# Optimization experiments

Measured on AMD Instinct MI355X. Metric: run time of the kernel, lower is better.

## Reference

```python
import jax, jax.numpy as jnp
import numpy as np

N_NODES = 65536


def gcn_conv(x, W, b, src, dst, n_nodes):
    """PyG GCNConv: symmetric-normalized aggregation with self-loops.
    out = D^{-1/2} (A + I) D^{-1/2} (x W) + b, deg counted on targets incl. self-loop.
    """
    h = x @ W  # [N, F_out]
    # in-degree including the self-loop
    deg = jnp.zeros((n_nodes,), dtype=x.dtype).at[dst].add(1.0) + 1.0
    dis = jax.lax.rsqrt(deg)  # deg^{-1/2}
    norm = dis[src] * dis[dst]  # [E]
    msg = h[src] * norm[:, None]  # [E, F_out] gathered+scaled messages
    agg = jax.ops.segment_sum(msg, dst, num_segments=n_nodes)
    agg = agg + h * (dis * dis)[:, None]  # self-loop contribution, norm = dis[i]^2
    return agg + b


def setup_inputs() -> dict:
    key = jax.random.key(0)
    k1, k2, k3, k4 = jax.random.split(key, 4)
    d_in, d_hid = 64, 64
    x = jax.random.normal(k1, (N_NODES, d_in), dtype=jnp.float32)
    edge_index = jax.random.randint(k2, (2, 1048576), 0, N_NODES, dtype=jnp.int64)
    s = 1.0 / np.sqrt(d_in)
    W1 = jax.random.normal(k3, (d_in, d_hid), dtype=jnp.float32) * s
    b1 = jnp.zeros((d_hid,), dtype=jnp.float32)
    W2 = jax.random.normal(k4, (d_hid, d_hid), dtype=jnp.float32) * s
    b2 = jnp.zeros((d_hid,), dtype=jnp.float32)
    return {"x": x, "edge_index": edge_index, "W1": W1, "b1": b1, "W2": W2, "b2": b2}


def reference(x, edge_index, W1, b1, W2, b2):
    src, dst = edge_index[0], edge_index[1]
    n = x.shape[0]
    h = jax.nn.relu(gcn_conv(x, W1, b1, src, dst, n))
    h = jax.nn.relu(gcn_conv(h, W2, b2, src, dst, n))
    return h
```

## Files before the change

kernel.cpp:

```cpp
#include <hip/hip_runtime.h>

#define FDIM 64
#define EPB  1024
#define BCAP 6144

typedef float nf4 __attribute__((ext_vector_type(4)));
typedef float nf2 __attribute__((ext_vector_type(2)));

__device__ __forceinline__ unsigned f2bf(float f) {
    unsigned u = __float_as_uint(f);
    u += 0x7fffu + ((u >> 16) & 1u);
    return u >> 16;
}
__device__ __forceinline__ float bflo(unsigned u) { return __uint_as_float(u << 16); }
__device__ __forceinline__ float bfhi(unsigned u) { return __uint_as_float(u & 0xffff0000u); }


__global__ __launch_bounds__(256) void k_coarse(const int* __restrict__ ei,
                                                int* __restrict__ cursorG,
                                                int* __restrict__ packed, int nE) {
    __shared__ int lh[256], gb[256], lc[256];
    int t = threadIdx.x;
    lh[t] = 0; lc[t] = 0;
    __syncthreads();
    int base = blockIdx.x * EPB;
    int bins[EPB / 256], vals[EPB / 256];
    #pragma unroll
    for (int i = 0; i < EPB / 256; ++i) {
        int e = base + i * 256 + t;
        if (e < nE) {
            int s = ei[e];
            int d = ei[nE + e];
            bins[i] = d >> 8;
            vals[i] = (s << 8) | (d & 255);
            atomicAdd(&lh[bins[i]], 1);
        } else {
            bins[i] = -1;
        }
    }
    __syncthreads();
    gb[t] = atomicAdd(&cursorG[t], lh[t]);
    __syncthreads();
    #pragma unroll
    for (int i = 0; i < EPB / 256; ++i) {
        int b = bins[i];
        if (b >= 0) {
            int p = gb[b] + atomicAdd(&lc[b], 1);
            if (p < BCAP) packed[b * BCAP + p] = vals[i];
        }
    }
}

__global__ __launch_bounds__(256) void k_fine(const int* __restrict__ packed,
                                              const int* __restrict__ cursorG,
                                              float* __restrict__ dis,
                                              int* __restrict__ rowStart,
                                              unsigned short* __restrict__ lenArr,
                                              unsigned short* __restrict__ sortedSrc,
                                              int n) {
    __shared__ int cnt[256], loc[256], lc[256];
    int t = threadIdx.x;
    int b = blockIdx.x;
    int lo = b * BCAP;
    int hi = lo + cursorG[b];
    cnt[t] = 0; lc[t] = 0;
    __syncthreads();
    for (int k = lo + t; k < hi; k += 256)
        atomicAdd(&cnt[packed[k] & 255], 1);
    __syncthreads();

    int c = cnt[t];
    int node = (b << 8) + t;
    dis[node]    = rsqrtf((float)c + 1.0f);
    lenArr[node] = (unsigned short)c;

    loc[t] = c;
    __syncthreads();
    #pragma unroll
    for (int off = 1; off < 256; off <<= 1) {
        int u = (t >= off) ? loc[t - off] : 0;
        __syncthreads();
        loc[t] += u;
        __syncthreads();
    }
    int excl = loc[t] - c;
    rowStart[node] = lo + excl;
    __syncthreads();
    loc[t] = excl;
    __syncthreads();

    for (int k = lo + t; k < hi; k += 256) {
        int v = packed[k];
        int dl = v & 255;
        int p = loc[dl] + atomicAdd(&lc[dl], 1);
        sortedSrc[lo + p] = (unsigned short)(v >> 8);
    }
}


__global__ __launch_bounds__(256) void k_gemm64s(const float* __restrict__ X,
                                                 const float* __restrict__ W,
                                                 const float* __restrict__ dis,
                                                 unsigned* __restrict__ Hb) {
    __shared__ float Ws[64 * 64];
    __shared__ float XsT[64 * 68];

    const int tid  = threadIdx.x;
    const int row0 = blockIdx.x * 64;

    for (int i = tid; i < 4096; i += 256) Ws[i] = W[i];
    for (int i = tid; i < 4096; i += 256) {
        int r = i >> 6, k = i & 63;
        XsT[k * 68 + r] = X[(row0 + r) * FDIM + k];
    }
    __syncthreads();

    const int tx = tid & 15;
    const int ty = tid >> 4;

    float4 acc0 = {0,0,0,0}, acc1 = {0,0,0,0}, acc2 = {0,0,0,0}, acc3 = {0,0,0,0};

    #pragma unroll
    for (int k = 0; k < 64; ++k) {
        float4 wv = *(const float4*)&Ws[k * 64 + tx * 4];
        float4 xv = *(const float4*)&XsT[k * 68 + ty * 4];
        acc0.x = fmaf(xv.x, wv.x, acc0.x); acc0.y = fmaf(xv.x, wv.y, acc0.y);
        acc0.z = fmaf(xv.x, wv.z, acc0.z); acc0.w = fmaf(xv.x, wv.w, acc0.w);
        acc1.x = fmaf(xv.y, wv.x, acc1.x); acc1.y = fmaf(xv.y, wv.y, acc1.y);
        acc1.z = fmaf(xv.y, wv.z, acc1.z); acc1.w = fmaf(xv.y, wv.w, acc1.w);
        acc2.x = fmaf(xv.z, wv.x, acc2.x); acc2.y = fmaf(xv.z, wv.y, acc2.y);
        acc2.z = fmaf(xv.z, wv.z, acc2.z); acc2.w = fmaf(xv.z, wv.w, acc2.w);
        acc3.x = fmaf(xv.w, wv.x, acc3.x); acc3.y = fmaf(xv.w, wv.y, acc3.y);
        acc3.z = fmaf(xv.w, wv.z, acc3.z); acc3.w = fmaf(xv.w, wv.w, acc3.w);
    }

    float d0 = dis[row0 + ty * 4 + 0];
    float d1 = dis[row0 + ty * 4 + 1];
    float d2 = dis[row0 + ty * 4 + 2];
    float d3 = dis[row0 + ty * 4 + 3];

    uint2* H2 = (uint2*)Hb;
    uint2 o;
    o.x = f2bf(acc0.x * d0) | (f2bf(acc0.y * d0) << 16);
    o.y = f2bf(acc0.z * d0) | (f2bf(acc0.w * d0) << 16);
    H2[(row0 + ty * 4 + 0) * 16 + tx] = o;
    o.x = f2bf(acc1.x * d1) | (f2bf(acc1.y * d1) << 16);
    o.y = f2bf(acc1.z * d1) | (f2bf(acc1.w * d1) << 16);
    H2[(row0 + ty * 4 + 1) * 16 + tx] = o;
    o.x = f2bf(acc2.x * d2) | (f2bf(acc2.y * d2) << 16);
    o.y = f2bf(acc2.z * d2) | (f2bf(acc2.w * d2) << 16);
    H2[(row0 + ty * 4 + 2) * 16 + tx] = o;
    o.x = f2bf(acc3.x * d3) | (f2bf(acc3.y * d3) << 16);
    o.y = f2bf(acc3.z * d3) | (f2bf(acc3.w * d3) << 16);
    H2[(row0 + ty * 4 + 3) * 16 + tx] = o;
}


__global__ __launch_bounds__(256) void k_aggemm(const unsigned* __restrict__ Hb1,
                                                const float* __restrict__ dis,
                                                const int* __restrict__ rowStart,
                                                const unsigned short* __restrict__ lenArr,
                                                const unsigned short* __restrict__ esrc,
                                                const float* __restrict__ bias,
                                                const float* __restrict__ W,
                                                unsigned* __restrict__ Hb2) {
    __shared__ float Ws[64 * 64];
    __shared__ float XsT[64 * 68];

    const int tid  = threadIdx.x;
    const int row0 = blockIdx.x * 64;

    for (int i = tid; i < 4096; i += 256) Ws[i] = W[i];

    const int fq = tid & 7;
    const int rr = tid >> 3;
    const uint4* H = (const uint4*)Hb1;
    const float4* b4 = (const float4*)bias;
    const float4 bb0 = b4[fq * 2];
    const float4 bb1 = b4[fq * 2 + 1];

    #pragma unroll
    for (int half = 0; half < 2; ++half) {
        const int r   = rr + half * 32;
        const int row = row0 + r;
        const int start = rowStart[row];
        const int end   = start + (int)lenArr[row];

        nf2 p0 = {0, 0}, p1 = {0, 0}, p2 = {0, 0}, p3 = {0, 0};
        int k = start;
        for (; k + 4 <= end; k += 4) {
            int s0 = (int)__builtin_nontemporal_load(&esrc[k]);
            int s1 = (int)__builtin_nontemporal_load(&esrc[k + 1]);
            int s2 = (int)__builtin_nontemporal_load(&esrc[k + 2]);
            int s3 = (int)__builtin_nontemporal_load(&esrc[k + 3]);
            uint4 v0 = H[s0 * 8 + fq];
            uint4 v1 = H[s1 * 8 + fq];
            uint4 v2 = H[s2 * 8 + fq];
            uint4 v3 = H[s3 * 8 + fq];
            p0 += (nf2){bflo(v0.x), bfhi(v0.x)}; p1 += (nf2){bflo(v0.y), bfhi(v0.y)};
            p2 += (nf2){bflo(v0.z), bfhi(v0.z)}; p3 += (nf2){bflo(v0.w), bfhi(v0.w)};
            p0 += (nf2){bflo(v1.x), bfhi(v1.x)}; p1 += (nf2){bflo(v1.y), bfhi(v1.y)};
            p2 += (nf2){bflo(v1.z), bfhi(v1.z)}; p3 += (nf2){bflo(v1.w), bfhi(v1.w)};
            p0 += (nf2){bflo(v2.x), bfhi(v2.x)}; p1 += (nf2){bflo(v2.y), bfhi(v2.y)};
            p2 += (nf2){bflo(v2.z), bfhi(v2.z)}; p3 += (nf2){bflo(v2.w), bfhi(v2.w)};
            p0 += (nf2){bflo(v3.x), bfhi(v3.x)}; p1 += (nf2){bflo(v3.y), bfhi(v3.y)};
            p2 += (nf2){bflo(v3.z), bfhi(v3.z)}; p3 += (nf2){bflo(v3.w), bfhi(v3.w)};
        }
        for (; k < end; ++k) {
            int s0 = (int)__builtin_nontemporal_load(&esrc[k]);
            uint4 v0 = H[s0 * 8 + fq];
            p0 += (nf2){bflo(v0.x), bfhi(v0.x)}; p1 += (nf2){bflo(v0.y), bfhi(v0.y)};
            p2 += (nf2){bflo(v0.z), bfhi(v0.z)}; p3 += (nf2){bflo(v0.w), bfhi(v0.w)};
        }

        uint4 sv = H[row * 8 + fq];
        float ds = dis[row];
        float* col = &XsT[(fq * 8) * 68 + r];
        col[0 * 68] = fmaxf(fmaf(p0.x + bflo(sv.x), ds, bb0.x), 0.f);
        col[1 * 68] = fmaxf(fmaf(p0.y + bfhi(sv.x), ds, bb0.y), 0.f);
        col[2 * 68] = fmaxf(fmaf(p1.x + bflo(sv.y), ds, bb0.z), 0.f);
        col[3 * 68] = fmaxf(fmaf(p1.y + bfhi(sv.y), ds, bb0.w), 0.f);
        col[4 * 68] = fmaxf(fmaf(p2.x + bflo(sv.z), ds, bb1.x), 0.f);
        col[5 * 68] = fmaxf(fmaf(p2.y + bfhi(sv.z), ds, bb1.y), 0.f);
        col[6 * 68] = fmaxf(fmaf(p3.x + bflo(sv.w), ds, bb1.z), 0.f);
        col[7 * 68] = fmaxf(fmaf(p3.y + bfhi(sv.w), ds, bb1.w), 0.f);
    }
    __syncthreads();

    const int tx = tid & 15;
    const int ty = tid >> 4;

    float4 acc0 = {0,0,0,0}, acc1 = {0,0,0,0}, acc2 = {0,0,0,0}, acc3 = {0,0,0,0};

    #pragma unroll
    for (int k = 0; k < 64; ++k) {
        float4 wv = *(const float4*)&Ws[k * 64 + tx * 4];
        float4 xv = *(const float4*)&XsT[k * 68 + ty * 4];
        acc0.x = fmaf(xv.x, wv.x, acc0.x); acc0.y = fmaf(xv.x, wv.y, acc0.y);
        acc0.z = fmaf(xv.x, wv.z, acc0.z); acc0.w = fmaf(xv.x, wv.w, acc0.w);
        acc1.x = fmaf(xv.y, wv.x, acc1.x); acc1.y = fmaf(xv.y, wv.y, acc1.y);
        acc1.z = fmaf(xv.y, wv.z, acc1.z); acc1.w = fmaf(xv.y, wv.w, acc1.w);
        acc2.x = fmaf(xv.z, wv.x, acc2.x); acc2.y = fmaf(xv.z, wv.y, acc2.y);
        acc2.z = fmaf(xv.z, wv.z, acc2.z); acc2.w = fmaf(xv.z, wv.w, acc2.w);
        acc3.x = fmaf(xv.w, wv.x, acc3.x); acc3.y = fmaf(xv.w, wv.y, acc3.y);
        acc3.z = fmaf(xv.w, wv.z, acc3.z); acc3.w = fmaf(xv.w, wv.w, acc3.w);
    }

    float d0 = dis[row0 + ty * 4 + 0];
    float d1 = dis[row0 + ty * 4 + 1];
    float d2 = dis[row0 + ty * 4 + 2];
    float d3 = dis[row0 + ty * 4 + 3];

    uint2* H2 = (uint2*)Hb2;
    uint2 o;
    o.x = f2bf(acc0.x * d0) | (f2bf(acc0.y * d0) << 16);
    o.y = f2bf(acc0.z * d0) | (f2bf(acc0.w * d0) << 16);
    H2[(row0 + ty * 4 + 0) * 16 + tx] = o;
    o.x = f2bf(acc1.x * d1) | (f2bf(acc1.y * d1) << 16);
    o.y = f2bf(acc1.z * d1) | (f2bf(acc1.w * d1) << 16);
    H2[(row0 + ty * 4 + 1) * 16 + tx] = o;
    o.x = f2bf(acc2.x * d2) | (f2bf(acc2.y * d2) << 16);
    o.y = f2bf(acc2.z * d2) | (f2bf(acc2.w * d2) << 16);
    H2[(row0 + ty * 4 + 2) * 16 + tx] = o;
    o.x = f2bf(acc3.x * d3) | (f2bf(acc3.y * d3) << 16);
    o.y = f2bf(acc3.z * d3) | (f2bf(acc3.w * d3) << 16);
    H2[(row0 + ty * 4 + 3) * 16 + tx] = o;
}


__global__ __launch_bounds__(256) void k_agg(const unsigned* __restrict__ Hb,
                                             const float* __restrict__ dis,
                                             const int* __restrict__ rowStart,
                                             const unsigned short* __restrict__ lenArr,
                                             const unsigned short* __restrict__ esrc,
                                             const float* __restrict__ bias,
                                             float* __restrict__ out) {
    const int tid = threadIdx.x;
    const int fq  = tid & 7;
    const int row = blockIdx.x * 32 + (tid >> 3);

    const int start = rowStart[row];
    const int end   = start + (int)lenArr[row];

    const uint4* H = (const uint4*)Hb;

    nf2 p0 = {0, 0}, p1 = {0, 0}, p2 = {0, 0}, p3 = {0, 0};

    int k = start;
    for (; k + 4 <= end; k += 4) {
        int s0 = (int)__builtin_nontemporal_load(&esrc[k]);
        int s1 = (int)__builtin_nontemporal_load(&esrc[k + 1]);
        int s2 = (int)__builtin_nontemporal_load(&esrc[k + 2]);
        int s3 = (int)__builtin_nontemporal_load(&esrc[k + 3]);
        uint4 v0 = H[s0 * 8 + fq];
        uint4 v1 = H[s1 * 8 + fq];
        uint4 v2 = H[s2 * 8 + fq];
        uint4 v3 = H[s3 * 8 + fq];
        p0 += (nf2){bflo(v0.x), bfhi(v0.x)}; p1 += (nf2){bflo(v0.y), bfhi(v0.y)};
        p2 += (nf2){bflo(v0.z), bfhi(v0.z)}; p3 += (nf2){bflo(v0.w), bfhi(v0.w)};
        p0 += (nf2){bflo(v1.x), bfhi(v1.x)}; p1 += (nf2){bflo(v1.y), bfhi(v1.y)};
        p2 += (nf2){bflo(v1.z), bfhi(v1.z)}; p3 += (nf2){bflo(v1.w), bfhi(v1.w)};
        p0 += (nf2){bflo(v2.x), bfhi(v2.x)}; p1 += (nf2){bflo(v2.y), bfhi(v2.y)};
        p2 += (nf2){bflo(v2.z), bfhi(v2.z)}; p3 += (nf2){bflo(v2.w), bfhi(v2.w)};
        p0 += (nf2){bflo(v3.x), bfhi(v3.x)}; p1 += (nf2){bflo(v3.y), bfhi(v3.y)};
        p2 += (nf2){bflo(v3.z), bfhi(v3.z)}; p3 += (nf2){bflo(v3.w), bfhi(v3.w)};
    }
    for (; k < end; ++k) {
        int s0 = (int)__builtin_nontemporal_load(&esrc[k]);
        uint4 v0 = H[s0 * 8 + fq];
        p0 += (nf2){bflo(v0.x), bfhi(v0.x)}; p1 += (nf2){bflo(v0.y), bfhi(v0.y)};
        p2 += (nf2){bflo(v0.z), bfhi(v0.z)}; p3 += (nf2){bflo(v0.w), bfhi(v0.w)};
    }

    uint4 sv = H[row * 8 + fq];
    float ds = dis[row];
    const float4* b4 = (const float4*)bias;
    float4 b0 = b4[fq * 2];
    float4 b1 = b4[fq * 2 + 1];

    nf4 r0, r1;
    r0.x = fmaxf(fmaf(p0.x + bflo(sv.x), ds, b0.x), 0.f);
    r0.y = fmaxf(fmaf(p0.y + bfhi(sv.x), ds, b0.y), 0.f);
    r0.z = fmaxf(fmaf(p1.x + bflo(sv.y), ds, b0.z), 0.f);
    r0.w = fmaxf(fmaf(p1.y + bfhi(sv.y), ds, b0.w), 0.f);
    r1.x = fmaxf(fmaf(p2.x + bflo(sv.z), ds, b1.x), 0.f);
    r1.y = fmaxf(fmaf(p2.y + bfhi(sv.z), ds, b1.y), 0.f);
    r1.z = fmaxf(fmaf(p3.x + bflo(sv.w), ds, b1.z), 0.f);
    r1.w = fmaxf(fmaf(p3.y + bfhi(sv.w), ds, b1.w), 0.f);

    nf4* O = (nf4*)out;
    __builtin_nontemporal_store(r0, &O[row * 16 + fq * 2]);
    __builtin_nontemporal_store(r1, &O[row * 16 + fq * 2 + 1]);
}


extern "C" void kernel_launch(void* const* d_in, const int* in_sizes, int n_in,
                              void* d_out, int out_size, void* d_ws, size_t ws_size,
                              hipStream_t stream) {
    const float* x  = (const float*)d_in[0];
    const int*   ei = (const int*)d_in[1];
    const float* W1 = (const float*)d_in[2];
    const float* b1 = (const float*)d_in[3];
    const float* W2 = (const float*)d_in[4];
    const float* b2 = (const float*)d_in[5];

    const int N = in_sizes[0] / FDIM;
    const int E = in_sizes[1] / 2;

    char* ws = (char*)d_ws;
    float*          dis       = (float*)(ws);
    int*            rowStart  = (int*)  (ws + 262144);
    unsigned short* lenArr    = (unsigned short*)(ws + 524288);
    int*            cursorG   = (int*)  (ws + 655360);
    unsigned short* sortedSrc = (unsigned short*)(ws + 656384);
    char*           heap      = ws + 656384 + 3145728;
    int*            packed    = (int*)heap;
    unsigned*       HSb1      = (unsigned*)heap;
    unsigned*       HSb2      = (unsigned*)(heap + 8388608);

    hipMemsetAsync(cursorG, 0, 256 * sizeof(int), stream);
    k_coarse<<<(E + EPB - 1) / EPB, 256, 0, stream>>>(ei, cursorG, packed, E);
    k_fine  <<<256, 256, 0, stream>>>(packed, cursorG, dis, rowStart, lenArr, sortedSrc, N);

    k_gemm64s<<<N / 64, 256, 0, stream>>>(x, W1, dis, HSb1);
    k_aggemm <<<N / 64, 256, 0, stream>>>(HSb1, dis, rowStart, lenArr, sortedSrc, b1, W2, HSb2);
    k_agg    <<<N / 32, 256, 0, stream>>>(HSb2, dis, rowStart, lenArr, sortedSrc, b2, (float*)d_out);
}
```

Baseline: 118.0 us.

## Decouple first GEMM from degree computation and fold memset into it

The first-layer GEMM no longer scales rows by deg^-1/2, so it can run before the edge sort. It also absorbs the cursor memset through an extra block, which removes one API call. The aggregation kernels now gather dis[src] per edge and multiply each message by it, and the self-loop term and output are scaled by the destination's dis. This cuts one dependency and one launch at the cost of an extra scalar gather and multiply per edge in both aggregation passes, and the workspace layout is reshuffled so packed no longer aliases H1.

```diff
diff --git a/kernel.cpp b/kernel.cpp
--- a/kernel.cpp
+++ b/kernel.cpp
@@ -14,6 +14,69 @@
 }
 __device__ __forceinline__ float bflo(unsigned u) { return __uint_as_float(u << 16); }
 __device__ __forceinline__ float bfhi(unsigned u) { return __uint_as_float(u & 0xffff0000u); }
+
+#define ACC4(v) \
+    p0 += (nf2){bflo((v).x), bfhi((v).x)}; p1 += (nf2){bflo((v).y), bfhi((v).y)}; \
+    p2 += (nf2){bflo((v).z), bfhi((v).z)}; p3 += (nf2){bflo((v).w), bfhi((v).w)};
+
+
+__global__ __launch_bounds__(256) void k_gemm64u(const float* __restrict__ X,
+                                                 const float* __restrict__ W,
+                                                 unsigned* __restrict__ Hb,
+                                                 int* __restrict__ cursorG,
+                                                 int nTiles) {
+    if ((int)blockIdx.x >= nTiles) {
+        if (threadIdx.x < 256) cursorG[threadIdx.x] = 0;
+        return;
+    }
+    __shared__ float Ws[64 * 64];
+    __shared__ float XsT[64 * 68];
+
+    const int tid  = threadIdx.x;
+    const int row0 = blockIdx.x * 64;
+
+    for (int i = tid; i < 4096; i += 256) Ws[i] = W[i];
+    for (int i = tid; i < 4096; i += 256) {
+        int r = i >> 6, k = i & 63;
+        XsT[k * 68 + r] = X[(row0 + r) * FDIM + k];
+    }
+    __syncthreads();
+
+    const int tx = tid & 15;
+    const int ty = tid >> 4;
+
+    float4 acc0 = {0,0,0,0}, acc1 = {0,0,0,0}, acc2 = {0,0,0,0}, acc3 = {0,0,0,0};
+
+    #pragma unroll
+    for (int k = 0; k < 64; ++k) {
+        float4 wv = *(const float4*)&Ws[k * 64 + tx * 4];
+        float4 xv = *(const float4*)&XsT[k * 68 + ty * 4];
+        acc0.x = fmaf(xv.x, wv.x, acc0.x); acc0.y = fmaf(xv.x, wv.y, acc0.y);
+        acc0.z = fmaf(xv.x, wv.z, acc0.z); acc0.w = fmaf(xv.x, wv.w, acc0.w);
+        acc1.x = fmaf(xv.y, wv.x, acc1.x); acc1.y = fmaf(xv.y, wv.y, acc1.y);
+        acc1.z = fmaf(xv.y, wv.z, acc1.z); acc1.w = fmaf(xv.y, wv.w, acc1.w);
+        acc2.x = fmaf(xv.z, wv.x, acc2.x); acc2.y = fmaf(xv.z, wv.y, acc2.y);
+        acc2.z = fmaf(xv.z, wv.z, acc2.z); acc2.w = fmaf(xv.z, wv.w, acc2.w);
+        acc3.x = fmaf(xv.w, wv.x, acc3.x); acc3.y = fmaf(xv.w, wv.y, acc3.y);
+        acc3.z = fmaf(xv.w, wv.z, acc3.z); acc3.w = fmaf(xv.w, wv.w, acc3.w);
+    }
+
+    uint2* H2 = (uint2*)Hb;
+    uint2 o;
+    o.x = f2bf(acc0.x) | (f2bf(acc0.y) << 16);
+    o.y = f2bf(acc0.z) | (f2bf(acc0.w) << 16);
+    H2[(row0 + ty * 4 + 0) * 16 + tx] = o;
+    o.x = f2bf(acc1.x) | (f2bf(acc1.y) << 16);
+    o.y = f2bf(acc1.z) | (f2bf(acc1.w) << 16);
+    H2[(row0 + ty * 4 + 1) * 16 + tx] = o;
+    o.x = f2bf(acc2.x) | (f2bf(acc2.y) << 16);
+    o.y = f2bf(acc2.z) | (f2bf(acc2.w) << 16);
+    H2[(row0 + ty * 4 + 2) * 16 + tx] = o;
+    o.x = f2bf(acc3.x) | (f2bf(acc3.y) << 16);
+    o.y = f2bf(acc3.z) | (f2bf(acc3.w) << 16);
+    H2[(row0 + ty * 4 + 3) * 16 + tx] = o;
+}
+
 
 
 __global__ __launch_bounds__(256) void k_coarse(const int* __restrict__ ei,
@@ -98,10 +161,14 @@
 }
 
 
-__global__ __launch_bounds__(256) void k_gemm64s(const float* __restrict__ X,
-                                                 const float* __restrict__ W,
-                                                 const float* __restrict__ dis,
-                                                 unsigned* __restrict__ Hb) {
+__global__ __launch_bounds__(256) void k_aggemm(const unsigned* __restrict__ Hb1,
+                                                const float* __restrict__ dis,
+                                                const int* __restrict__ rowStart,
+                                                const unsigned short* __restrict__ lenArr,
+                                                const unsigned short* __restrict__ esrc,
+                                                const float* __restrict__ bias,
+                                                const float* __restrict__ W,
+                                                unsigned* __restrict__ Hb2) {
     __shared__ float Ws[64 * 64];
     __shared__ float XsT[64 * 68];
 
@@ -109,9 +176,71 @@
     const int row0 = blockIdx.x * 64;
 
     for (int i = tid; i < 4096; i += 256) Ws[i] = W[i];
-    for (int i = tid; i < 4096; i += 256) {
-        int r = i >> 6, k = i & 63;
-        XsT[k * 68 + r] = X[(row0 + r) * FDIM + k];
+
+    const int fq = tid & 7;
+    const int rr = tid >> 3;
+    const uint4* H = (const uint4*)Hb1;
+    const float4* b4 = (const float4*)bias;
+    const float4 bb0 = b4[fq * 2];
+    const float4 bb1 = b4[fq * 2 + 1];
+
+    #pragma unroll
+    for (int half = 0; half < 2; ++half) {
+        const int r   = rr + half * 32;
+        const int row = row0 + r;
+        const int start = rowStart[row];
+        const int end   = start + (int)lenArr[row];
+
+        nf2 p0 = {0, 0}, p1 = {0, 0}, p2 = {0, 0}, p3 = {0, 0};
+        int k = start;
+        for (; k + 4 <= end; k += 4) {
+            int s0 = (int)__builtin_nontemporal_load(&esrc[k]);
+            int s1 = (int)__builtin_nontemporal_load(&esrc[k + 1]);
+            int s2 = (int)__builtin_nontemporal_load(&esrc[k + 2]);
+            int s3 = (int)__builtin_nontemporal_load(&esrc[k + 3]);
+            uint4 v0 = H[s0 * 8 + fq];
+            uint4 v1 = H[s1 * 8 + fq];
+            uint4 v2 = H[s2 * 8 + fq];
+            uint4 v3 = H[s3 * 8 + fq];
+            float w0 = dis[s0], w1 = dis[s1], w2 = dis[s2], w3 = dis[s3];
+            p0 += (nf2){bflo(v0.x) * w0, bfhi(v0.x) * w0};
+            p1 += (nf2){bflo(v0.y) * w0, bfhi(v0.y) * w0};
+            p2 += (nf2){bflo(v0.z) * w0, bfhi(v0.z) * w0};
+            p3 += (nf2){bflo(v0.w) * w0, bfhi(v0.w) * w0};
+            p0 += (nf2){bflo(v1.x) * w1, bfhi(v1.x) * w1};
+            p1 += (nf2){bflo(v1.y) * w1, bfhi(v1.y) * w1};
+            p2 += (nf2){bflo(v1.z) * w1, bfhi(v1.z) * w1};
+            p3 += (nf2){bflo(v1.w) * w1, bfhi(v1.w) * w1};
+            p0 += (nf2){bflo(v2.x) * w2, bfhi(v2.x) * w2};
+            p1 += (nf2){bflo(v2.y) * w2, bfhi(v2.y) * w2};
+            p2 += (nf2){bflo(v2.z) * w2, bfhi(v2.z) * w2};
+            p3 += (nf2){bflo(v2.w) * w2, bfhi(v2.w) * w2};
+            p0 += (nf2){bflo(v3.x) * w3, bfhi(v3.x) * w3};
+            p1 += (nf2){bflo(v3.y) * w3, bfhi(v3.y) * w3};
+            p2 += (nf2){bflo(v3.z) * w3, bfhi(v3.z) * w3};
+            p3 += (nf2){bflo(v3.w) * w3, bfhi(v3.w) * w3};
+        }
+        for (; k < end; ++k) {
+            int s0 = (int)__builtin_nontemporal_load(&esrc[k]);
+            uint4 v0 = H[s0 * 8 + fq];
+            float w0 = dis[s0];
+            p0 += (nf2){bflo(v0.x) * w0, bfhi(v0.x) * w0};
+            p1 += (nf2){bflo(v0.y) * w0, bfhi(v0.y) * w0};
+            p2 += (nf2){bflo(v0.z) * w0, bfhi(v0.z) * w0};
+            p3 += (nf2){bflo(v0.w) * w0, bfhi(v0.w) * w0};
+        }
+
+        uint4 sv = H[row * 8 + fq];
+        float ds = dis[row];
+        float* col = &XsT[(fq * 8) * 68 + r];
+        col[0 * 68] = fmaxf(fmaf(fmaf(bflo(sv.x), ds, p0.x), ds, bb0.x), 0.f);
+        col[1 * 68] = fmaxf(fmaf(fmaf(bfhi(sv.x), ds, p0.y), ds, bb0.y), 0.f);
+        col[2 * 68] = fmaxf(fmaf(fmaf(bflo(sv.y), ds, p1.x), ds, bb0.z), 0.f);
+        col[3 * 68] = fmaxf(fmaf(fmaf(bfhi(sv.y), ds, p1.y), ds, bb0.w), 0.f);
+        col[4 * 68] = fmaxf(fmaf(fmaf(bflo(sv.z), ds, p2.x), ds, bb1.x), 0.f);
+        col[5 * 68] = fmaxf(fmaf(fmaf(bfhi(sv.z), ds, p2.y), ds, bb1.y), 0.f);
+        col[6 * 68] = fmaxf(fmaf(fmaf(bflo(sv.w), ds, p3.x), ds, bb1.z), 0.f);
+        col[7 * 68] = fmaxf(fmaf(fmaf(bfhi(sv.w), ds, p3.y), ds, bb1.w), 0.f);
     }
     __syncthreads();
 
@@ -134,136 +263,19 @@
         acc3.z = fmaf(xv.w, wv.z, acc3.z); acc3.w = fmaf(xv.w, wv.w, acc3.w);
     }
 
-    float d0 = dis[row0 + ty * 4 + 0];
-    float d1 = dis[row0 + ty * 4 + 1];
-    float d2 = dis[row0 + ty * 4 + 2];
-    float d3 = dis[row0 + ty * 4 + 3];
-
-    uint2* H2 = (uint2*)Hb;
-    uint2 o;
-    o.x = f2bf(acc0.x * d0) | (f2bf(acc0.y * d0) << 16);
-    o.y = f2bf(acc0.z * d0) | (f2bf(acc0.w * d0) << 16);
-    H2[(row0 + ty * 4 + 0) * 16 + tx] = o;
-    o.x = f2bf(acc1.x * d1) | (f2bf(acc1.y * d1) << 16);
-    o.y = f2bf(acc1.z * d1) | (f2bf(acc1.w * d1) << 16);
-    H2[(row0 + ty * 4 + 1) * 16 + tx] = o;
-    o.x = f2bf(acc2.x * d2) | (f2bf(acc2.y * d2) << 16);
-    o.y = f2bf(acc2.z * d2) | (f2bf(acc2.w * d2) << 16);
-    H2[(row0 + ty * 4 + 2) * 16 + tx] = o;
-    o.x = f2bf(acc3.x * d3) | (f2bf(acc3.y * d3) << 16);
-    o.y = f2bf(acc3.z * d3) | (f2bf(acc3.w * d3) << 16);
-    H2[(row0 + ty * 4 + 3) * 16 + tx] = o;
-}
-
-
-__global__ __launch_bounds__(256) void k_aggemm(const unsigned* __restrict__ Hb1,
-                                                const float* __restrict__ dis,
-                                                const int* __restrict__ rowStart,
-                                                const unsigned short* __restrict__ lenArr,
-                                                const unsigned short* __restrict__ esrc,
-                                                const float* __restrict__ bias,
-                                                const float* __restrict__ W,
-                                                unsigned* __restrict__ Hb2) {
-    __shared__ float Ws[64 * 64];
-    __shared__ float XsT[64 * 68];
-
-    const int tid  = threadIdx.x;
-    const int row0 = blockIdx.x * 64;
-
-    for (int i = tid; i < 4096; i += 256) Ws[i] = W[i];
-
-    const int fq = tid & 7;
-    const int rr = tid >> 3;
-    const uint4* H = (const uint4*)Hb1;
-    const float4* b4 = (const float4*)bias;
-    const float4 bb0 = b4[fq * 2];
-    const float4 bb1 = b4[fq * 2 + 1];
-
-    #pragma unroll
-    for (int half = 0; half < 2; ++half) {
-        const int r   = rr + half * 32;
-        const int row = row0 + r;
-        const int start = rowStart[row];
-        const int end   = start + (int)lenArr[row];
-
-        nf2 p0 = {0, 0}, p1 = {0, 0}, p2 = {0, 0}, p3 = {0, 0};
-        int k = start;
-        for (; k + 4 <= end; k += 4) {
-            int s0 = (int)__builtin_nontemporal_load(&esrc[k]);
-            int s1 = (int)__builtin_nontemporal_load(&esrc[k + 1]);
-            int s2 = (int)__builtin_nontemporal_load(&esrc[k + 2]);
-            int s3 = (int)__builtin_nontemporal_load(&esrc[k + 3]);
-            uint4 v0 = H[s0 * 8 + fq];
-            uint4 v1 = H[s1 * 8 + fq];
-            uint4 v2 = H[s2 * 8 + fq];
-            uint4 v3 = H[s3 * 8 + fq];
-            p0 += (nf2){bflo(v0.x), bfhi(v0.x)}; p1 += (nf2){bflo(v0.y), bfhi(v0.y)};
-            p2 += (nf2){bflo(v0.z), bfhi(v0.z)}; p3 += (nf2){bflo(v0.w), bfhi(v0.w)};
-            p0 += (nf2){bflo(v1.x), bfhi(v1.x)}; p1 += (nf2){bflo(v1.y), bfhi(v1.y)};
-            p2 += (nf2){bflo(v1.z), bfhi(v1.z)}; p3 += (nf2){bflo(v1.w), bfhi(v1.w)};
-            p0 += (nf2){bflo(v2.x), bfhi(v2.x)}; p1 += (nf2){bflo(v2.y), bfhi(v2.y)};
-            p2 += (nf2){bflo(v2.z), bfhi(v2.z)}; p3 += (nf2){bflo(v2.w), bfhi(v2.w)};
-            p0 += (nf2){bflo(v3.x), bfhi(v3.x)}; p1 += (nf2){bflo(v3.y), bfhi(v3.y)};
-            p2 += (nf2){bflo(v3.z), bfhi(v3.z)}; p3 += (nf2){bflo(v3.w), bfhi(v3.w)};
-        }
-        for (; k < end; ++k) {
-            int s0 = (int)__builtin_nontemporal_load(&esrc[k]);
-            uint4 v0 = H[s0 * 8 + fq];
-            p0 += (nf2){bflo(v0.x), bfhi(v0.x)}; p1 += (nf2){bflo(v0.y), bfhi(v0.y)};
-            p2 += (nf2){bflo(v0.z), bfhi(v0.z)}; p3 += (nf2){bflo(v0.w), bfhi(v0.w)};
-        }
-
-        uint4 sv = H[row * 8 + fq];
-        float ds = dis[row];
-        float* col = &XsT[(fq * 8) * 68 + r];
-        col[0 * 68] = fmaxf(fmaf(p0.x + bflo(sv.x), ds, bb0.x), 0.f);
-        col[1 * 68] = fmaxf(fmaf(p0.y + bfhi(sv.x), ds, bb0.y), 0.f);
-        col[2 * 68] = fmaxf(fmaf(p1.x + bflo(sv.y), ds, bb0.z), 0.f);
-        col[3 * 68] = fmaxf(fmaf(p1.y + bfhi(sv.y), ds, bb0.w), 0.f);
-        col[4 * 68] = fmaxf(fmaf(p2.x + bflo(sv.z), ds, bb1.x), 0.f);
-        col[5 * 68] = fmaxf(fmaf(p2.y + bfhi(sv.z), ds, bb1.y), 0.f);
-        col[6 * 68] = fmaxf(fmaf(p3.x + bflo(sv.w), ds, bb1.z), 0.f);
-        col[7 * 68] = fmaxf(fmaf(p3.y + bfhi(sv.w), ds, bb1.w), 0.f);
-    }
-    __syncthreads();
-
-    const int tx = tid & 15;
-    const int ty = tid >> 4;
-
-    float4 acc0 = {0,0,0,0}, acc1 = {0,0,0,0}, acc2 = {0,0,0,0}, acc3 = {0,0,0,0};
-
-    #pragma unroll
-    for (int k = 0; k < 64; ++k) {
-        float4 wv = *(const float4*)&Ws[k * 64 + tx * 4];
-        float4 xv = *(const float4*)&XsT[k * 68 + ty * 4];
-        acc0.x = fmaf(xv.x, wv.x, acc0.x); acc0.y = fmaf(xv.x, wv.y, acc0.y);
-        acc0.z = fmaf(xv.x, wv.z, acc0.z); acc0.w = fmaf(xv.x, wv.w, acc0.w);
-        acc1.x = fmaf(xv.y, wv.x, acc1.x); acc1.y = fmaf(xv.y, wv.y, acc1.y);
-        acc1.z = fmaf(xv.y, wv.z, acc1.z); acc1.w = fmaf(xv.y, wv.w, acc1.w);
-        acc2.x = fmaf(xv.z, wv.x, acc2.x); acc2.y = fmaf(xv.z, wv.y, acc2.y);
-        acc2.z = fmaf(xv.z, wv.z, acc2.z); acc2.w = fmaf(xv.z, wv.w, acc2.w);
-        acc3.x = fmaf(xv.w, wv.x, acc3.x); acc3.y = fmaf(xv.w, wv.y, acc3.y);
-        acc3.z = fmaf(xv.w, wv.z, acc3.z); acc3.w = fmaf(xv.w, wv.w, acc3.w);
-    }
-
-    float d0 = dis[row0 + ty * 4 + 0];
-    float d1 = dis[row0 + ty * 4 + 1];
-    float d2 = dis[row0 + ty * 4 + 2];
-    float d3 = dis[row0 + ty * 4 + 3];
-
     uint2* H2 = (uint2*)Hb2;
     uint2 o;
-    o.x = f2bf(acc0.x * d0) | (f2bf(acc0.y * d0) << 16);
-    o.y = f2bf(acc0.z * d0) | (f2bf(acc0.w * d0) << 16);
+    o.x = f2bf(acc0.x) | (f2bf(acc0.y) << 16);
+    o.y = f2bf(acc0.z) | (f2bf(acc0.w) << 16);
     H2[(row0 + ty * 4 + 0) * 16 + tx] = o;
-    o.x = f2bf(acc1.x * d1) | (f2bf(acc1.y * d1) << 16);
-    o.y = f2bf(acc1.z * d1) | (f2bf(acc1.w * d1) << 16);
+    o.x = f2bf(acc1.x) | (f2bf(acc1.y) << 16);
+    o.y = f2bf(acc1.z) | (f2bf(acc1.w) << 16);
     H2[(row0 + ty * 4 + 1) * 16 + tx] = o;
-    o.x = f2bf(acc2.x * d2) | (f2bf(acc2.y * d2) << 16);
-    o.y = f2bf(acc2.z * d2) | (f2bf(acc2.w * d2) << 16);
+    o.x = f2bf(acc2.x) | (f2bf(acc2.y) << 16);
+    o.y = f2bf(acc2.z) | (f2bf(acc2.w) << 16);
     H2[(row0 + ty * 4 + 2) * 16 + tx] = o;
-    o.x = f2bf(acc3.x * d3) | (f2bf(acc3.y * d3) << 16);
-    o.y = f2bf(acc3.z * d3) | (f2bf(acc3.w * d3) << 16);
+    o.x = f2bf(acc3.x) | (f2bf(acc3.y) << 16);
+    o.y = f2bf(acc3.z) | (f2bf(acc3.w) << 16);
     H2[(row0 + ty * 4 + 3) * 16 + tx] = o;
 }
 
@@ -296,20 +308,32 @@
         uint4 v1 = H[s1 * 8 + fq];
         uint4 v2 = H[s2 * 8 + fq];
         uint4 v3 = H[s3 * 8 + fq];
-        p0 += (nf2){bflo(v0.x), bfhi(v0.x)}; p1 += (nf2){bflo(v0.y), bfhi(v0.y)};
-        p2 += (nf2){bflo(v0.z), bfhi(v0.z)}; p3 += (nf2){bflo(v0.w), bfhi(v0.w)};
-        p0 += (nf2){bflo(v1.x), bfhi(v1.x)}; p1 += (nf2){bflo(v1.y), bfhi(v1.y)};
-        p2 += (nf2){bflo(v1.z), bfhi(v1.z)}; p3 += (nf2){bflo(v1.w), bfhi(v1.w)};
-        p0 += (nf2){bflo(v2.x), bfhi(v2.x)}; p1 += (nf2){bflo(v2.y), bfhi(v2.y)};
-        p2 += (nf2){bflo(v2.z), bfhi(v2.z)}; p3 += (nf2){bflo(v2.w), bfhi(v2.w)};
-        p0 += (nf2){bflo(v3.x), bfhi(v3.x)}; p1 += (nf2){bflo(v3.y), bfhi(v3.y)};
-        p2 += (nf2){bflo(v3.z), bfhi(v3.z)}; p3 += (nf2){bflo(v3.w), bfhi(v3.w)};
+        float w0 = dis[s0], w1 = dis[s1], w2 = dis[s2], w3 = dis[s3];
+        p0 += (nf2){bflo(v0.x) * w0, bfhi(v0.x) * w0};
+        p1 += (nf2){bflo(v0.y) * w0, bfhi(v0.y) * w0};
+        p2 += (nf2){bflo(v0.z) * w0, bfhi(v0.z) * w0};
+        p3 += (nf2){bflo(v0.w) * w0, bfhi(v0.w) * w0};
+        p0 += (nf2){bflo(v1.x) * w1, bfhi(v1.x) * w1};
+        p1 += (nf2){bflo(v1.y) * w1, bfhi(v1.y) * w1};
+        p2 += (nf2){bflo(v1.z) * w1, bfhi(v1.z) * w1};
+        p3 += (nf2){bflo(v1.w) * w1, bfhi(v1.w) * w1};
+        p0 += (nf2){bflo(v2.x) * w2, bfhi(v2.x) * w2};
+        p1 += (nf2){bflo(v2.y) * w2, bfhi(v2.y) * w2};
+        p2 += (nf2){bflo(v2.z) * w2, bfhi(v2.z) * w2};
+        p3 += (nf2){bflo(v2.w) * w2, bfhi(v2.w) * w2};
+        p0 += (nf2){bflo(v3.x) * w3, bfhi(v3.x) * w3};
+        p1 += (nf2){bflo(v3.y) * w3, bfhi(v3.y) * w3};
+        p2 += (nf2){bflo(v3.z) * w3, bfhi(v3.z) * w3};
+        p3 += (nf2){bflo(v3.w) * w3, bfhi(v3.w) * w3};
     }
     for (; k < end; ++k) {
         int s0 = (int)__builtin_nontemporal_load(&esrc[k]);
         uint4 v0 = H[s0 * 8 + fq];
-        p0 += (nf2){bflo(v0.x), bfhi(v0.x)}; p1 += (nf2){bflo(v0.y), bfhi(v0.y)};
-        p2 += (nf2){bflo(v0.z), bfhi(v0.z)}; p3 += (nf2){bflo(v0.w), bfhi(v0.w)};
+        float w0 = dis[s0];
+        p0 += (nf2){bflo(v0.x) * w0, bfhi(v0.x) * w0};
+        p1 += (nf2){bflo(v0.y) * w0, bfhi(v0.y) * w0};
+        p2 += (nf2){bflo(v0.z) * w0, bfhi(v0.z) * w0};
+        p3 += (nf2){bflo(v0.w) * w0, bfhi(v0.w) * w0};
     }
 
     uint4 sv = H[row * 8 + fq];
@@ -319,14 +343,14 @@
     float4 b1 = b4[fq * 2 + 1];
 
     nf4 r0, r1;
-    r0.x = fmaxf(fmaf(p0.x + bflo(sv.x), ds, b0.x), 0.f);
-    r0.y = fmaxf(fmaf(p0.y + bfhi(sv.x), ds, b0.y), 0.f);
-    r0.z = fmaxf(fmaf(p1.x + bflo(sv.y), ds, b0.z), 0.f);
-    r0.w = fmaxf(fmaf(p1.y + bfhi(sv.y), ds, b0.w), 0.f);
-    r1.x = fmaxf(fmaf(p2.x + bflo(sv.z), ds, b1.x), 0.f);
-    r1.y = fmaxf(fmaf(p2.y + bfhi(sv.z), ds, b1.y), 0.f);
-    r1.z = fmaxf(fmaf(p3.x + bflo(sv.w), ds, b1.z), 0.f);
-    r1.w = fmaxf(fmaf(p3.y + bfhi(sv.w), ds, b1.w), 0.f);
+    r0.x = fmaxf(fmaf(fmaf(bflo(sv.x), ds, p0.x), ds, b0.x), 0.f);
+    r0.y = fmaxf(fmaf(fmaf(bfhi(sv.x), ds, p0.y), ds, b0.y), 0.f);
+    r0.z = fmaxf(fmaf(fmaf(bflo(sv.y), ds, p1.x), ds, b0.z), 0.f);
+    r0.w = fmaxf(fmaf(fmaf(bfhi(sv.y), ds, p1.y), ds, b0.w), 0.f);
+    r1.x = fmaxf(fmaf(fmaf(bflo(sv.z), ds, p2.x), ds, b1.x), 0.f);
+    r1.y = fmaxf(fmaf(fmaf(bfhi(sv.z), ds, p2.y), ds, b1.y), 0.f);
+    r1.z = fmaxf(fmaf(fmaf(bflo(sv.w), ds, p3.x), ds, b1.z), 0.f);
+    r1.w = fmaxf(fmaf(fmaf(bfhi(sv.w), ds, p3.y), ds, b1.w), 0.f);
 
     nf4* O = (nf4*)out;
     __builtin_nontemporal_store(r0, &O[row * 16 + fq * 2]);
@@ -354,15 +378,15 @@
     int*            cursorG   = (int*)  (ws + 655360);
     unsigned short* sortedSrc = (unsigned short*)(ws + 656384);
     char*           heap      = ws + 656384 + 3145728;
-    int*            packed    = (int*)heap;
+    int*            packed    = (int*)(heap + 8388608);
     unsigned*       HSb1      = (unsigned*)heap;
-    unsigned*       HSb2      = (unsigned*)(heap + 8388608);
-
-    hipMemsetAsync(cursorG, 0, 256 * sizeof(int), stream);
+    unsigned*       HSb2      = (unsigned*)(heap + 8388608 + 6291456);
+
+    const int nTiles = N / 64;
+
+    k_gemm64u<<<nTiles + 1, 256, 0, stream>>>(x, W1, HSb1, cursorG, nTiles);
     k_coarse<<<(E + EPB - 1) / EPB, 256, 0, stream>>>(ei, cursorG, packed, E);
     k_fine  <<<256, 256, 0, stream>>>(packed, cursorG, dis, rowStart, lenArr, sortedSrc, N);
-
-    k_gemm64s<<<N / 64, 256, 0, stream>>>(x, W1, dis, HSb1);
-    k_aggemm <<<N / 64, 256, 0, stream>>>(HSb1, dis, rowStart, lenArr, sortedSrc, b1, W2, HSb2);
-    k_agg    <<<N / 32, 256, 0, stream>>>(HSb2, dis, rowStart, lenArr, sortedSrc, b2, (float*)d_out);
-}
+    k_aggemm<<<nTiles, 256, 0, stream>>>(HSb1, dis, rowStart, lenArr, sortedSrc, b1, W2, HSb2);
+    k_agg   <<<N / 32, 256, 0, stream>>>(HSb2, dis, rowStart, lenArr, sortedSrc, b2, (float*)d_out);
+}
```

After: 123.2 us. +4.3%, slower.
